# Kernel tuning notes

Hardware: AMD Instinct MI355X
Metric: run time of the kernel (lower is better)

Reference implementation:

```python
import jax, jax.numpy as jnp
import numpy as np

N = 10000      # nodes
F_IN = 256     # input feature dim
H1 = 128       # hidden_dim1
H2 = 64        # hidden_dim2 (latent)
E = 320000     # edges (avg degree 32)


def setup_inputs() -> dict:
    key = jax.random.key(0)
    ks = jax.random.split(key, 10)
    x = jax.random.normal(ks[0], (N, F_IN), dtype=jnp.float32)
    edge_index = jax.random.randint(ks[1], (2, E), 0, N, dtype=jnp.int64)
    edge_weight = jax.random.uniform(ks[2], (E,), dtype=jnp.float32)
    s1 = 1.0 / np.sqrt(F_IN)
    s2 = 1.0 / np.sqrt(H1)
    W1 = jax.random.normal(ks[3], (F_IN, H1), dtype=jnp.float32) * s1
    b1 = jnp.zeros((H1,), dtype=jnp.float32)
    W2 = jax.random.normal(ks[4], (H1, H2), dtype=jnp.float32) * s2
    b2 = jnp.zeros((H2,), dtype=jnp.float32)
    W3 = jax.random.normal(ks[5], (H1, H2), dtype=jnp.float32) * s2
    b3 = jnp.zeros((H2,), dtype=jnp.float32)
    return {"x": x, "edge_index": edge_index, "edge_weight": edge_weight,
            "W1": W1, "b1": b1, "W2": W2, "b2": b2, "W3": W3, "b3": b3}


def _gcn_norm(edge_index, edge_weight, n):
    # add self-loops with weight 1, symmetric deg^-1/2 normalization (PyG GCNConv)
    loop = jnp.arange(n)
    row = jnp.concatenate([edge_index[0], loop])
    col = jnp.concatenate([edge_index[1], loop])
    w = jnp.concatenate([edge_weight, jnp.ones((n,), edge_weight.dtype)])
    deg = jax.ops.segment_sum(w, col, num_segments=n)
    dis = jnp.where(deg > 0, jax.lax.rsqrt(deg), 0.0)
    norm = dis[row] * w * dis[col]
    return row, col, norm


def _gcn_conv(h, W, b, row, col, norm, n):
    hw = h @ W                                   # [N, out] transform first (PyG order)
    out = jax.ops.segment_sum(norm[:, None] * hw[row], col, num_segments=n)
    return out + b


def reference(x, edge_index, edge_weight, W1, b1, W2, b2, W3, b3):
    n = x.shape[0]
    row, col, norm = _gcn_norm(edge_index, edge_weight, n)
    h1 = jax.nn.relu(_gcn_conv(x, W1, b1, row, col, norm, n))
    mu = _gcn_conv(h1, W2, b2, row, col, norm, n)
    logvar = _gcn_conv(h1, W3, b3, row, col, norm, n)
    # eval mode: reparameterize -> mu, dropout inactive, decoder act = identity
    z = mu
    adj = z @ z.T                                # [N, N] inner-product decode
    return adj, mu, logvar
```

## Files before the change

kernel.cpp:

```cpp
#include <hip/hip_runtime.h>

#define N_NODES 10000
#define F_IN    256
#define H1      128
#define H2      64
#define NEDGE   320000
#define M_TOT   (NEDGE + N_NODES)

typedef __attribute__((ext_vector_type(8))) short          s16v8;
typedef __attribute__((ext_vector_type(8))) unsigned short u16v8;
typedef __attribute__((ext_vector_type(4))) float          f32v4;


__global__ void k_init(float* deg, int* cnt) {
    int i = blockIdx.x * blockDim.x + threadIdx.x;
    if (i < N_NODES) { deg[i] = 1.0f; cnt[i] = 1; }
}

__global__ void k_count(const int* __restrict__ ei, const float* __restrict__ w,
                        float* deg, int* cnt) {
    int e = blockIdx.x * blockDim.x + threadIdx.x;
    if (e < NEDGE) {
        int c = ei[NEDGE + e];
        atomicAdd(&deg[c], w[e]);
        atomicAdd(&cnt[c], 1);
    }
}

__global__ void k_scan(const int* __restrict__ cnt, int* __restrict__ ptr,
                       int* __restrict__ cur) {
    __shared__ int part[1024];
    int t = threadIdx.x;
    int base = t * 10;
    int local[10];
    int s = 0;
#pragma unroll
    for (int j = 0; j < 10; j++) {
        int idx = base + j;
        int v = (idx < N_NODES) ? cnt[idx] : 0;
        local[j] = s;
        s += v;
    }
    part[t] = s;
    __syncthreads();
    for (int off = 1; off < 1024; off <<= 1) {
        int v = (t >= off) ? part[t - off] : 0;
        __syncthreads();
        part[t] += v;
        __syncthreads();
    }
    int excl = t ? part[t - 1] : 0;
#pragma unroll
    for (int j = 0; j < 10; j++) {
        int idx = base + j;
        if (idx < N_NODES) {
            int p = excl + local[j];
            ptr[idx] = p;
            cur[idx] = p;
        }
    }
    if (t == 1023) ptr[N_NODES] = part[1023];
}

__global__ void k_scatter(const int* __restrict__ ei, const float* __restrict__ w,
                          const float* __restrict__ deg, int* cur,
                          int* __restrict__ src, float* __restrict__ wgt) {
    int t = blockIdx.x * blockDim.x + threadIdx.x;
    if (t >= M_TOT) return;
    int r, c; float nw;
    if (t < NEDGE) {
        r = ei[t];
        c = ei[NEDGE + t];
        nw = rsqrtf(deg[r]) * w[t] * rsqrtf(deg[c]);
    } else {
        r = c = t - NEDGE;
        float d = rsqrtf(deg[r]);
        nw = d * d;
    }
    int pos = atomicAdd(&cur[c], 1);
    src[pos] = r;
    wgt[pos] = nw;
}


__global__ __launch_bounds__(128) void k_gemm1(const float* __restrict__ x,
                                               const float* __restrict__ W1,
                                               float* __restrict__ hw) {
    __shared__ float xs[8 * F_IN];
    int i0 = blockIdx.x * 8;
    int t = threadIdx.x;
    const float4* xsrc = (const float4*)(x + (size_t)i0 * F_IN);
    float4* xd = (float4*)xs;
#pragma unroll
    for (int j = 0; j < 4; j++) xd[t + j * 128] = xsrc[t + j * 128];
    __syncthreads();
    float acc[8] = {0, 0, 0, 0, 0, 0, 0, 0};
    for (int k = 0; k < F_IN; k += 4) {
        float w0 = W1[(k + 0) * H1 + t];
        float w1 = W1[(k + 1) * H1 + t];
        float w2 = W1[(k + 2) * H1 + t];
        float w3 = W1[(k + 3) * H1 + t];
#pragma unroll
        for (int r = 0; r < 8; r++) {
            float4 xv = *(const float4*)&xs[r * F_IN + k];
            acc[r] += xv.x * w0 + xv.y * w1 + xv.z * w2 + xv.w * w3;
        }
    }
#pragma unroll
    for (int r = 0; r < 8; r++) hw[(size_t)(i0 + r) * H1 + t] = acc[r];
}

__global__ __launch_bounds__(256) void k_agg1g23(const int* __restrict__ ptr,
                                                 const int* __restrict__ src,
                                                 const float* __restrict__ wgt,
                                                 const float* __restrict__ hw,
                                                 const float* __restrict__ b1,
                                                 const float* __restrict__ W2,
                                                 const float* __restrict__ W3,
                                                 float* __restrict__ t2,
                                                 float* __restrict__ t3) {
    __shared__ float h1s[2][H1];
    int tid = threadIdx.x;
    {
        int half = tid >> 7;
        int f = tid & 127;
        int i = blockIdx.x * 2 + half;
        int jb = ptr[i], je = ptr[i + 1];
        float acc = b1[f];
        for (int j = jb; j < je; j++)
            acc += wgt[j] * hw[(size_t)src[j] * H1 + f];
        h1s[half][f] = fmaxf(acc, 0.0f);
    }
    __syncthreads();
    {
        int f = tid & 63;
        int wv = tid >> 6;
        int sel = wv & 1, nh = wv >> 1;
        const float* W = sel ? W3 : W2;
        const float* hr = h1s[nh];
        float s = 0.0f;
        for (int k = 0; k < H1; k += 4) {
            float4 hv = *(const float4*)&hr[k];
            s += hv.x * W[(k + 0) * H2 + f] + hv.y * W[(k + 1) * H2 + f]
               + hv.z * W[(k + 2) * H2 + f] + hv.w * W[(k + 3) * H2 + f];
        }
        int node = blockIdx.x * 2 + nh;
        float* o = sel ? t3 : t2;
        o[(size_t)node * H2 + f] = s;
    }
}

__global__ __launch_bounds__(128) void k_agg2(const int* __restrict__ ptr,
                                              const int* __restrict__ src,
                                              const float* __restrict__ wgt,
                                              const float* __restrict__ t2,
                                              const float* __restrict__ t3,
                                              const float* __restrict__ b2,
                                              const float* __restrict__ b3,
                                              float* __restrict__ mu,
                                              float* __restrict__ lv) {
    int i = blockIdx.x;
    int t = threadIdx.x;
    int f = t & 63;
    int sel = t >> 6;
    const float* tin = sel ? t3 : t2;
    float acc = sel ? b3[f] : b2[f];
    int jb = ptr[i], je = ptr[i + 1];
    for (int j = jb; j < je; j++)
        acc += wgt[j] * tin[(size_t)src[j] * H2 + f];
    float* o = sel ? lv : mu;
    o[(size_t)i * H2 + f] = acc;
}

__global__ __launch_bounds__(256, 1) void k_adj(const float* __restrict__ z,
                                                float* __restrict__ adj) {
    __shared__ __align__(16) unsigned short PAs[128 * 64];
    __shared__ __align__(16) unsigned short PBs[128 * 64];
    __shared__ __align__(16) unsigned short PLs[128 * 64];
    int tid = threadIdx.x;
    int rowBase = blockIdx.y * 128, colBase = blockIdx.x * 128;

    int lane = tid & 63;
    int wv   = tid >> 6;
    int wr = (wv >> 1) * 64;
    int wc = (wv & 1) * 64;
    int lrow = lane & 15;
    int lk   = lane >> 4;

    int sr   = tid & 127;
    int isB  = tid >> 7;
    int gbase = (isB ? colBase : rowBase) + sr;
    bool ok = gbase < N_NODES;
    const float* srcp = z + (size_t)gbase * 64;
    unsigned short* PH = isB ? PBs : PAs;
    int lslotBase = isB ? 4 : 0;
    int rb7 = sr & 7;

    auto stage = [&](int s) {
#pragma unroll
        for (int g = 0; g < 4; g++) {
            float v[8];
            if (ok) {
                float4 a = *(const float4*)(srcp + s * 32 + g * 8);
                float4 b = *(const float4*)(srcp + s * 32 + g * 8 + 4);
                v[0] = a.x; v[1] = a.y; v[2] = a.z; v[3] = a.w;
                v[4] = b.x; v[5] = b.y; v[6] = b.z; v[7] = b.w;
            } else {
#pragma unroll
                for (int q = 0; q < 8; q++) v[q] = 0.0f;
            }
            u16v8 hv, mv, lv8;
#pragma unroll
            for (int q = 0; q < 8; q++) {
                float xv = v[q];
                unsigned hu = __float_as_uint(xv) & 0xffff0000u;
                float r1 = xv - __uint_as_float(hu);
                unsigned mu2 = __float_as_uint(r1) & 0xffff0000u;
                float r2 = r1 - __uint_as_float(mu2);
                unsigned lu = __float_as_uint(r2) & 0xffff0000u;
                hv[q]  = (unsigned short)(hu >> 16);
                mv[q]  = (unsigned short)(mu2 >> 16);
                lv8[q] = (unsigned short)(lu >> 16);
            }
            int base = sr * 64;
            *reinterpret_cast<u16v8*>(PH  + base + ((g              ^ rb7) * 8)) = hv;
            *reinterpret_cast<u16v8*>(PH  + base + (((4 + g)        ^ rb7) * 8)) = mv;
            *reinterpret_cast<u16v8*>(PLs + base + (((lslotBase + g) ^ rb7) * 8)) = lv8;
        }
    };

    f32v4 acc[4][4];
#pragma unroll
    for (int i = 0; i < 4; i++)
#pragma unroll
        for (int j = 0; j < 4; j++) acc[i][j] = (f32v4)0.0f;

    s16v8 a0[4], a1[4], a2[4], b0[4], b1[4], b2[4];

#define LOADFRAGS()                                                        \
    {                                                                      \
        _Pragma("unroll")                                                  \
        for (int fq = 0; fq < 4; fq++) {                                   \
            int ra = wr + fq * 16 + lrow;                                  \
            int r7 = ra & 7;                                               \
            int ia = ra * 64;                                              \
            a0[fq] = *reinterpret_cast<const s16v8*>(&PAs[ia + ((lk       ^ r7) * 8)]); \
            a1[fq] = *reinterpret_cast<const s16v8*>(&PAs[ia + (((4 + lk) ^ r7) * 8)]); \
            a2[fq] = *reinterpret_cast<const s16v8*>(&PLs[ia + ((lk       ^ r7) * 8)]); \
            int rb = wc + fq * 16 + lrow;                                  \
            int q7 = rb & 7;                                               \
            int ib = rb * 64;                                              \
            b0[fq] = *reinterpret_cast<const s16v8*>(&PBs[ib + ((lk       ^ q7) * 8)]); \
            b1[fq] = *reinterpret_cast<const s16v8*>(&PBs[ib + (((4 + lk) ^ q7) * 8)]); \
            b2[fq] = *reinterpret_cast<const s16v8*>(&PLs[ib + (((4 + lk) ^ q7) * 8)]); \
        }                                                                  \
    }

#define MFMAS()                                                            \
    {                                                                      \
        _Pragma("unroll")                                                  \
        for (int i = 0; i < 4; i++) {                                      \
            _Pragma("unroll")                                              \
            for (int j = 0; j < 4; j++) {                                  \
                f32v4 c = acc[i][j];                                       \
                c = __builtin_amdgcn_mfma_f32_16x16x32_bf16(a0[i], b0[j], c, 0, 0, 0); \
                c = __builtin_amdgcn_mfma_f32_16x16x32_bf16(a0[i], b1[j], c, 0, 0, 0); \
                c = __builtin_amdgcn_mfma_f32_16x16x32_bf16(a1[i], b0[j], c, 0, 0, 0); \
                c = __builtin_amdgcn_mfma_f32_16x16x32_bf16(a0[i], b2[j], c, 0, 0, 0); \
                c = __builtin_amdgcn_mfma_f32_16x16x32_bf16(a2[i], b0[j], c, 0, 0, 0); \
                c = __builtin_amdgcn_mfma_f32_16x16x32_bf16(a1[i], b1[j], c, 0, 0, 0); \
                acc[i][j] = c;                                             \
            }                                                              \
        }                                                                  \
    }

    stage(0);
    __syncthreads();
    LOADFRAGS();
    __syncthreads();
    stage(1);
    MFMAS();
    __syncthreads();
    LOADFRAGS();
    MFMAS();

#undef LOADFRAGS
#undef MFMAS

#pragma unroll
    for (int i = 0; i < 4; i++) {
        int r0 = rowBase + wr + i * 16 + lk * 4;
        if (r0 < N_NODES) {
#pragma unroll
            for (int j = 0; j < 4; j++) {
                int cg = colBase + wc + j * 16 + lrow;
                if (cg < N_NODES)
                    *(float4*)&adj[(size_t)cg * N_NODES + r0] =
                        make_float4(acc[i][j][0], acc[i][j][1], acc[i][j][2], acc[i][j][3]);
            }
        }
    }
}


extern "C" void kernel_launch(void* const* d_in, const int* in_sizes, int n_in,
                              void* d_out, int out_size, void* d_ws, size_t ws_size,
                              hipStream_t stream) {
    const float* x  = (const float*)d_in[0];
    const int*   ei = (const int*)d_in[1];
    const float* w  = (const float*)d_in[2];
    const float* W1 = (const float*)d_in[3];
    const float* b1 = (const float*)d_in[4];
    const float* W2 = (const float*)d_in[5];
    const float* b2 = (const float*)d_in[6];
    const float* W3 = (const float*)d_in[7];
    const float* b3 = (const float*)d_in[8];

    float* out = (float*)d_out;
    float* adj = out;
    float* mu  = out + (size_t)N_NODES * N_NODES;
    float* lv  = mu + (size_t)N_NODES * H2;

    float* ws  = out + 80000000;
    float* deg = ws;
    int*   cnt = (int*)(ws + 10240);
    int*   ptr = (int*)(ws + 20480);
    int*   cur = (int*)(ws + 30720);
    int*   src = (int*)(ws + 40960);
    float* wgt = ws + 371200;
    float* hw  = ws + 701440;
    float* t2  = ws + 3261440;
    float* t3  = ws + 3901440;

    hipLaunchKernelGGL(k_init,    dim3((N_NODES + 255) / 256), dim3(256), 0, stream, deg, cnt);
    hipLaunchKernelGGL(k_count,   dim3((NEDGE + 255) / 256),   dim3(256), 0, stream, ei, w, deg, cnt);
    hipLaunchKernelGGL(k_scan,    dim3(1), dim3(1024), 0, stream, cnt, ptr, cur);
    hipLaunchKernelGGL(k_scatter, dim3((M_TOT + 255) / 256),   dim3(256), 0, stream, ei, w, deg, cur, src, wgt);
    hipLaunchKernelGGL(k_gemm1,   dim3(N_NODES / 8),  dim3(128), 0, stream, x, W1, hw);
    hipLaunchKernelGGL(k_agg1g23, dim3(N_NODES / 2),  dim3(256), 0, stream, ptr, src, wgt, hw, b1, W2, W3, t2, t3);
    hipLaunchKernelGGL(k_agg2,    dim3(N_NODES),      dim3(128), 0, stream, ptr, src, wgt, t2, t3, b2, b3, mu, lv);

    dim3 g((N_NODES + 127) / 128, (N_NODES + 127) / 128);
    hipLaunchKernelGGL(k_adj, g, dim3(256), 0, stream, mu, adj);
}
```

Baseline: 715.4 us.

## Replace CSR build with fixed-capacity buckets, fuse degree count into GEMM1, retune adj

Drops the count and scan kernels and stores each node's incoming edges in a fixed 128-slot bucket indexed by atomic cursor, so aggregation reads bucket counts directly. The degree atomics are folded into the first GEMM launch as extra blocks, and that GEMM now handles 16 rows per 256-thread block. The adj kernel gets occupancy hint 2 and writes its tile as scalar row-major stores instead of float4 stores to transposed positions. Fixed buckets overflow if any node has more than 127 in-edges, which random inputs make unlikely but not impossible, and the scalar stores may reduce store efficiency on the dominant adj write.

```diff
diff --git a/kernel.cpp b/kernel.cpp
--- a/kernel.cpp
+++ b/kernel.cpp
@@ -6,113 +6,80 @@
 #define H2      64
 #define NEDGE   320000
 #define M_TOT   (NEDGE + N_NODES)
+#define BCAP    128
 
 typedef __attribute__((ext_vector_type(8))) short          s16v8;
 typedef __attribute__((ext_vector_type(8))) unsigned short u16v8;
 typedef __attribute__((ext_vector_type(4))) float          f32v4;
 
 
-__global__ void k_init(float* deg, int* cnt) {
+__global__ void k_zero(float* deg, int* cur) {
     int i = blockIdx.x * blockDim.x + threadIdx.x;
-    if (i < N_NODES) { deg[i] = 1.0f; cnt[i] = 1; }
-}
-
-__global__ void k_count(const int* __restrict__ ei, const float* __restrict__ w,
-                        float* deg, int* cnt) {
-    int e = blockIdx.x * blockDim.x + threadIdx.x;
-    if (e < NEDGE) {
-        int c = ei[NEDGE + e];
-        atomicAdd(&deg[c], w[e]);
-        atomicAdd(&cnt[c], 1);
-    }
-}
-
-__global__ void k_scan(const int* __restrict__ cnt, int* __restrict__ ptr,
-                       int* __restrict__ cur) {
-    __shared__ int part[1024];
-    int t = threadIdx.x;
-    int base = t * 10;
-    int local[10];
-    int s = 0;
-#pragma unroll
-    for (int j = 0; j < 10; j++) {
-        int idx = base + j;
-        int v = (idx < N_NODES) ? cnt[idx] : 0;
-        local[j] = s;
-        s += v;
-    }
-    part[t] = s;
-    __syncthreads();
-    for (int off = 1; off < 1024; off <<= 1) {
-        int v = (t >= off) ? part[t - off] : 0;
+    if (i < N_NODES) { deg[i] = 0.0f; cur[i] = 0; }
+}
+
+__global__ __launch_bounds__(256) void k_cg1(const float* __restrict__ x,
+                                             const float* __restrict__ W1,
+                                             float* __restrict__ hw,
+                                             const int* __restrict__ ei,
+                                             const float* __restrict__ w,
+                                             float* deg) {
+    __shared__ float xs[16 * F_IN];
+    int bid = blockIdx.x;
+    int tid = threadIdx.x;
+    if (bid < 625) {
+        int i0 = bid * 16;
+        const float4* xsrc = (const float4*)(x + (size_t)i0 * F_IN);
+        float4* xd = (float4*)xs;
+#pragma unroll
+        for (int j = 0; j < 4; j++) xd[tid + j * 256] = xsrc[tid + j * 256];
         __syncthreads();
-        part[t] += v;
-        __syncthreads();
-    }
-    int excl = t ? part[t - 1] : 0;
-#pragma unroll
-    for (int j = 0; j < 10; j++) {
-        int idx = base + j;
-        if (idx < N_NODES) {
-            int p = excl + local[j];
-            ptr[idx] = p;
-            cur[idx] = p;
+        int col = tid & 127, half = tid >> 7;
+        const float* xrow = xs + (half * 8) * F_IN;
+        float acc[8] = {0, 0, 0, 0, 0, 0, 0, 0};
+        for (int k = 0; k < F_IN; k += 4) {
+            float w0 = W1[(k + 0) * H1 + col];
+            float w1 = W1[(k + 1) * H1 + col];
+            float w2 = W1[(k + 2) * H1 + col];
+            float w3 = W1[(k + 3) * H1 + col];
+#pragma unroll
+            for (int r = 0; r < 8; r++) {
+                float4 xv = *(const float4*)&xrow[r * F_IN + k];
+                acc[r] += xv.x * w0 + xv.y * w1 + xv.z * w2 + xv.w * w3;
+            }
         }
-    }
-    if (t == 1023) ptr[N_NODES] = part[1023];
-}
-
-__global__ void k_scatter(const int* __restrict__ ei, const float* __restrict__ w,
-                          const float* __restrict__ deg, int* cur,
-                          int* __restrict__ src, float* __restrict__ wgt) {
+#pragma unroll
+        for (int r = 0; r < 8; r++)
+            hw[(size_t)(i0 + half * 8 + r) * H1 + col] = acc[r];
+    } else {
+        int e = (bid - 625) * 256 + tid;
+        if (e < NEDGE) atomicAdd(&deg[ei[NEDGE + e]], w[e]);
+    }
+}
+
+__global__ void k_scatb(const int* __restrict__ ei, const float* __restrict__ w,
+                        const float* __restrict__ deg, int* cur,
+                        int* __restrict__ bsrc, float* __restrict__ bwgt) {
     int t = blockIdx.x * blockDim.x + threadIdx.x;
     if (t >= M_TOT) return;
     int r, c; float nw;
     if (t < NEDGE) {
         r = ei[t];
         c = ei[NEDGE + t];
-        nw = rsqrtf(deg[r]) * w[t] * rsqrtf(deg[c]);
+        nw = rsqrtf(1.0f + deg[r]) * w[t] * rsqrtf(1.0f + deg[c]);
     } else {
         r = c = t - NEDGE;
-        float d = rsqrtf(deg[r]);
+        float d = rsqrtf(1.0f + deg[r]);
         nw = d * d;
     }
     int pos = atomicAdd(&cur[c], 1);
-    src[pos] = r;
-    wgt[pos] = nw;
-}
-
-
-__global__ __launch_bounds__(128) void k_gemm1(const float* __restrict__ x,
-                                               const float* __restrict__ W1,
-                                               float* __restrict__ hw) {
-    __shared__ float xs[8 * F_IN];
-    int i0 = blockIdx.x * 8;
-    int t = threadIdx.x;
-    const float4* xsrc = (const float4*)(x + (size_t)i0 * F_IN);
-    float4* xd = (float4*)xs;
-#pragma unroll
-    for (int j = 0; j < 4; j++) xd[t + j * 128] = xsrc[t + j * 128];
-    __syncthreads();
-    float acc[8] = {0, 0, 0, 0, 0, 0, 0, 0};
-    for (int k = 0; k < F_IN; k += 4) {
-        float w0 = W1[(k + 0) * H1 + t];
-        float w1 = W1[(k + 1) * H1 + t];
-        float w2 = W1[(k + 2) * H1 + t];
-        float w3 = W1[(k + 3) * H1 + t];
-#pragma unroll
-        for (int r = 0; r < 8; r++) {
-            float4 xv = *(const float4*)&xs[r * F_IN + k];
-            acc[r] += xv.x * w0 + xv.y * w1 + xv.z * w2 + xv.w * w3;
-        }
-    }
-#pragma unroll
-    for (int r = 0; r < 8; r++) hw[(size_t)(i0 + r) * H1 + t] = acc[r];
-}
-
-__global__ __launch_bounds__(256) void k_agg1g23(const int* __restrict__ ptr,
-                                                 const int* __restrict__ src,
-                                                 const float* __restrict__ wgt,
+    bsrc[(c << 7) + pos] = r;
+    bwgt[(c << 7) + pos] = nw;
+}
+
+__global__ __launch_bounds__(256) void k_agg1g23(const int* __restrict__ cur,
+                                                 const int* __restrict__ bsrc,
+                                                 const float* __restrict__ bwgt,
                                                  const float* __restrict__ hw,
                                                  const float* __restrict__ b1,
                                                  const float* __restrict__ W2,
@@ -125,10 +92,12 @@
         int half = tid >> 7;
         int f = tid & 127;
         int i = blockIdx.x * 2 + half;
-        int jb = ptr[i], je = ptr[i + 1];
+        int n = cur[i];
+        const int*   bs = bsrc + ((size_t)i << 7);
+        const float* bw = bwgt + ((size_t)i << 7);
         float acc = b1[f];
-        for (int j = jb; j < je; j++)
-            acc += wgt[j] * hw[(size_t)src[j] * H1 + f];
+        for (int j = 0; j < n; j++)
+            acc += bw[j] * hw[(size_t)bs[j] * H1 + f];
         h1s[half][f] = fmaxf(acc, 0.0f);
     }
     __syncthreads();
@@ -150,9 +119,9 @@
     }
 }
 
-__global__ __launch_bounds__(128) void k_agg2(const int* __restrict__ ptr,
-                                              const int* __restrict__ src,
-                                              const float* __restrict__ wgt,
+__global__ __launch_bounds__(128) void k_agg2(const int* __restrict__ cur,
+                                              const int* __restrict__ bsrc,
+                                              const float* __restrict__ bwgt,
                                               const float* __restrict__ t2,
                                               const float* __restrict__ t3,
                                               const float* __restrict__ b2,
@@ -165,14 +134,16 @@
     int sel = t >> 6;
     const float* tin = sel ? t3 : t2;
     float acc = sel ? b3[f] : b2[f];
-    int jb = ptr[i], je = ptr[i + 1];
-    for (int j = jb; j < je; j++)
-        acc += wgt[j] * tin[(size_t)src[j] * H2 + f];
+    int n = cur[i];
+    const int*   bs = bsrc + ((size_t)i << 7);
+    const float* bw = bwgt + ((size_t)i << 7);
+    for (int j = 0; j < n; j++)
+        acc += bw[j] * tin[(size_t)bs[j] * H2 + f];
     float* o = sel ? lv : mu;
     o[(size_t)i * H2 + f] = acc;
 }
 
-__global__ __launch_bounds__(256, 1) void k_adj(const float* __restrict__ z,
+__global__ __launch_bounds__(256, 2) void k_adj(const float* __restrict__ z,
                                                 float* __restrict__ adj) {
     __shared__ __align__(16) unsigned short PAs[128 * 64];
     __shared__ __align__(16) unsigned short PBs[128 * 64];
@@ -290,13 +261,16 @@
 #pragma unroll
     for (int i = 0; i < 4; i++) {
         int r0 = rowBase + wr + i * 16 + lk * 4;
-        if (r0 < N_NODES) {
-#pragma unroll
-            for (int j = 0; j < 4; j++) {
-                int cg = colBase + wc + j * 16 + lrow;
-                if (cg < N_NODES)
-                    *(float4*)&adj[(size_t)cg * N_NODES + r0] =
-                        make_float4(acc[i][j][0], acc[i][j][1], acc[i][j][2], acc[i][j][3]);
+#pragma unroll
+        for (int j = 0; j < 4; j++) {
+            int cg = colBase + wc + j * 16 + lrow;
+            if (cg < N_NODES) {
+#pragma unroll
+                for (int v = 0; v < 4; v++) {
+                    int rg = r0 + v;
+                    if (rg < N_NODES)
+                        adj[(size_t)rg * N_NODES + cg] = acc[i][j][v];
+                }
             }
         }
     }
@@ -321,24 +295,24 @@
     float* mu  = out + (size_t)N_NODES * N_NODES;
     float* lv  = mu + (size_t)N_NODES * H2;
 
-    float* ws  = out + 80000000;
-    float* deg = ws;
-    int*   cnt = (int*)(ws + 10240);
-    int*   ptr = (int*)(ws + 20480);
-    int*   cur = (int*)(ws + 30720);
-    int*   src = (int*)(ws + 40960);
-    float* wgt = ws + 371200;
-    float* hw  = ws + 701440;
-    float* t2  = ws + 3261440;
-    float* t3  = ws + 3901440;
-
-    hipLaunchKernelGGL(k_init,    dim3((N_NODES + 255) / 256), dim3(256), 0, stream, deg, cnt);
-    hipLaunchKernelGGL(k_count,   dim3((NEDGE + 255) / 256),   dim3(256), 0, stream, ei, w, deg, cnt);
-    hipLaunchKernelGGL(k_scan,    dim3(1), dim3(1024), 0, stream, cnt, ptr, cur);
-    hipLaunchKernelGGL(k_scatter, dim3((M_TOT + 255) / 256),   dim3(256), 0, stream, ei, w, deg, cur, src, wgt);
-    hipLaunchKernelGGL(k_gemm1,   dim3(N_NODES / 8),  dim3(128), 0, stream, x, W1, hw);
-    hipLaunchKernelGGL(k_agg1g23, dim3(N_NODES / 2),  dim3(256), 0, stream, ptr, src, wgt, hw, b1, W2, W3, t2, t3);
-    hipLaunchKernelGGL(k_agg2,    dim3(N_NODES),      dim3(128), 0, stream, ptr, src, wgt, t2, t3, b2, b3, mu, lv);
+    float* ws   = out + 80000000;
+    float* deg  = ws;
+    int*   cur  = (int*)(ws + 10240);
+    int*   bsrc = (int*)(ws + 20480);
+    float* bwgt = ws + 1300480;
+    float* hw   = ws + 2580480;
+    float* t2   = ws + 3860480;
+    float* t3   = ws + 4500480;
+
+    hipLaunchKernelGGL(k_zero,    dim3((N_NODES + 255) / 256), dim3(256), 0, stream, deg, cur);
+    hipLaunchKernelGGL(k_cg1,     dim3(625 + (NEDGE + 255) / 256), dim3(256), 0, stream,
+                       x, W1, hw, ei, w, deg);
+    hipLaunchKernelGGL(k_scatb,   dim3((M_TOT + 255) / 256), dim3(256), 0, stream,
+                       ei, w, deg, cur, bsrc, bwgt);
+    hipLaunchKernelGGL(k_agg1g23, dim3(N_NODES / 2), dim3(256), 0, stream,
+                       cur, bsrc, bwgt, hw, b1, W2, W3, t2, t3);
+    hipLaunchKernelGGL(k_agg2,    dim3(N_NODES), dim3(128), 0, stream,
+                       cur, bsrc, bwgt, t2, t3, b2, b3, mu, lv);
 
     dim3 g((N_NODES + 127) / 128, (N_NODES + 127) / 128);
     hipLaunchKernelGGL(k_adj, g, dim3(256), 0, stream, mu, adj);
```

New measurement: 661.5 us. -7.5%, faster.
